# Kernel tuning notes

Measured on AMD Instinct MI355X. Metric: run time of the kernel, lower is better.

The kernel has to match this reference:

```python
import jax, jax.numpy as jnp
import numpy as np

GRID = 3


def setup_inputs() -> dict:
    key = jax.random.key(0)
    k1, k2, k3 = jax.random.split(key, 3)
    b, c, h, w = 8, 64, 128, 128
    h0, w0 = 64, 64
    x = jax.random.normal(k1, (b, c, h, w), dtype=jnp.float32)
    depth = jax.random.normal(k2, (b, GRID * 4 * c, h0, w0), dtype=jnp.float32)
    depth_ori = jax.random.uniform(k3, (b, 1, h, w), dtype=jnp.float32)
    return {"x": x, "depth": depth, "depth_ori": depth_ori}


def reference(x, depth, depth_ori):
    b, c, h, w = x.shape
    # self.dc = Sigmoid, then bilinear upsample (align_corners=False -> half-pixel,
    # matching jax.image.resize 'bilinear')
    d = jax.nn.sigmoid(depth)
    d = jax.image.resize(d, (b, d.shape[1], h, w), method="bilinear")
    d = d.reshape(b, GRID, 4 * c, h, w)
    # depth-weighted triangular interpolation weights, clamped at 0
    rd = jnp.arange(GRID, dtype=x.dtype).reshape(1, GRID, 1, 1)
    rd = jnp.maximum(1.0 - jnp.abs(rd - depth_ori * GRID), 0.0)  # (b, GRID, h, w)
    d = (d * rd[:, :, None]).sum(axis=1)            # (b, 4*c, h, w)
    d = d.reshape(b, 4, 4, c // 4, h, w)
    eye = jnp.eye(4, dtype=x.dtype).reshape(1, 4, 4, 1, 1, 1)
    mat = d + eye                                   # per-pixel 4x4 mixing matrix
    xr = x.reshape(b, 1, 4, c // 4, h, w)
    out = (mat * xr).sum(axis=2)                    # contract over inner 4-axis
    return out.reshape(b, c, h, w)
```

## Files before the change

### kernel.cpp

```cpp
#include <hip/hip_runtime.h>


__device__ __forceinline__ float sigmoid_fast(float v) {
    float e = __builtin_amdgcn_exp2f(v * -1.44269504088896340736f);
    return __builtin_amdgcn_rcpf(1.0f + e);
}

__global__ __launch_bounds__(256) void seblock_kernel(
    const float* __restrict__ x,
    const float* __restrict__ depth,
    const float* __restrict__ dori,
    float* __restrict__ out)
{
    const int t  = blockIdx.x * 256 + threadIdx.x;
    const int n  = t & 63;
    const int m  = (t >> 6) & 63;
    const int oc = (t >> 12) & 63;
    const int b  = t >> 18;
    const int i  = oc >> 4;
    const int k  = oc & 15;

    const int h0 = m << 1, w0 = n << 1;

    const int rm = (m > 0)  ? m - 1 : 0;
    const int rp = (m < 63) ? m + 1 : 63;

    float dv[3][4][3];
    #pragma unroll
    for (int g = 0; g < 3; ++g) {
        #pragma unroll
        for (int j = 0; j < 4; ++j) {
            const float* dp = depth + ((size_t)b * 768 + (g * 256 + i * 64 + j * 16 + k)) * 4096 + n;
            dv[g][j][0] = dp[rm * 64];
            dv[g][j][1] = dp[m  * 64];
            dv[g][j][2] = dp[rp * 64];
        }
    }

    const float* dop = dori + ((size_t)b * 128 + h0) * 128 + w0;
    const float2 q0 = *reinterpret_cast<const float2*>(dop);
    const float2 q1 = *reinterpret_cast<const float2*>(dop + 128);
    const float z[4] = { q0.x * 3.0f, q0.y * 3.0f, q1.x * 3.0f, q1.y * 3.0f };

    float xs[4][4];
    #pragma unroll
    for (int j = 0; j < 4; ++j) {
        const float* xp = x + (((size_t)b * 64 + (j * 16 + k)) * 128 + h0) * 128 + w0;
        const float2 a = *reinterpret_cast<const float2*>(xp);
        const float2 c = *reinterpret_cast<const float2*>(xp + 128);
        xs[j][0] = a.x; xs[j][1] = a.y; xs[j][2] = c.x; xs[j][3] = c.y;
    }

    float acc[4] = { xs[i][0], xs[i][1], xs[i][2], xs[i][3] };

    #pragma unroll
    for (int g = 0; g < 3; ++g) {
        float rdw[4];
        #pragma unroll
        for (int p = 0; p < 4; ++p)
            rdw[p] = fmaxf(1.0f - fabsf((float)g - z[p]), 0.0f);

        #pragma unroll
        for (int j = 0; j < 4; ++j) {
            const float a0 = sigmoid_fast(dv[g][j][0]);
            const float a1 = sigmoid_fast(dv[g][j][1]);
            const float a2 = sigmoid_fast(dv[g][j][2]);

            const float vt = fmaf(0.25f, a0, 0.75f * a1);
            const float vb = fmaf(0.25f, a2, 0.75f * a1);

            const float vtm = __shfl_up(vt, 1);
            const float vtp = __shfl_down(vt, 1);
            const float vbm = __shfl_up(vb, 1);
            const float vbp = __shfl_down(vb, 1);

            const float u0 = fmaf(0.25f, vtm, 0.75f * vt);
            const float u1 = fmaf(0.25f, vtp, 0.75f * vt);
            const float u2 = fmaf(0.25f, vbm, 0.75f * vb);
            const float u3 = fmaf(0.25f, vbp, 0.75f * vb);

            acc[0] = fmaf(rdw[0] * u0, xs[j][0], acc[0]);
            acc[1] = fmaf(rdw[1] * u1, xs[j][1], acc[1]);
            acc[2] = fmaf(rdw[2] * u2, xs[j][2], acc[2]);
            acc[3] = fmaf(rdw[3] * u3, xs[j][3], acc[3]);
        }
    }

    float* op = out + (((size_t)b * 64 + oc) * 128 + h0) * 128 + w0;
    *reinterpret_cast<float2*>(op)       = make_float2(acc[0], acc[1]);
    *reinterpret_cast<float2*>(op + 128) = make_float2(acc[2], acc[3]);
}

extern "C" void kernel_launch(void* const* d_in, const int* in_sizes, int n_in,
                              void* d_out, int out_size, void* d_ws, size_t ws_size,
                              hipStream_t stream) {
    const float* x     = (const float*)d_in[0];
    const float* depth = (const float*)d_in[1];
    const float* dori  = (const float*)d_in[2];
    float* out = (float*)d_out;

    seblock_kernel<<<8192, 256, 0, stream>>>(x, depth, dori, out);
}
```

Baseline: 183.7 us.

## Slide each wave down 8 rows, reusing sigmoids and using packed half math

Each wavefront now handles 8 consecutive low-res rows for one channel/batch. It keeps sigmoid values for three depth rows in registers and slides the window, so each depth row is loaded and passed through sigmoid once instead of three times. The next row is prefetched while the current one is computed. Vertical and horizontal interpolation run in packed fp16 with half the shuffles, and the grid drops from 8192 to 1024 blocks with a min-occupancy launch bound. The fp16 interpolation adds rounding error, and fewer blocks plus higher register pressure may limit latency hiding.

```diff
diff --git a/kernel.cpp b/kernel.cpp
--- a/kernel.cpp
+++ b/kernel.cpp
@@ -1,4 +1,5 @@
 #include <hip/hip_runtime.h>
+#include <hip/hip_fp16.h>
 
 
 __device__ __forceinline__ float sigmoid_fast(float v) {
@@ -6,89 +7,118 @@
     return __builtin_amdgcn_rcpf(1.0f + e);
 }
 
-__global__ __launch_bounds__(256) void seblock_kernel(
+#define NCH 12
+
+__global__ __launch_bounds__(256, 4) void seblock_kernel(
     const float* __restrict__ x,
     const float* __restrict__ depth,
     const float* __restrict__ dori,
     float* __restrict__ out)
 {
-    const int t  = blockIdx.x * 256 + threadIdx.x;
-    const int n  = t & 63;
-    const int m  = (t >> 6) & 63;
-    const int oc = (t >> 12) & 63;
-    const int b  = t >> 18;
+    const int lane = threadIdx.x & 63;
+    const int wsub = __builtin_amdgcn_readfirstlane(threadIdx.x >> 6);
+    const int wid  = (blockIdx.x << 2) | wsub;
+    const int mt = wid & 7;
+    const int oc = (wid >> 3) & 63;
+    const int b  = wid >> 9;
     const int i  = oc >> 4;
     const int k  = oc & 15;
+    const int m0 = mt << 3;
 
-    const int h0 = m << 1, w0 = n << 1;
+    int cofs[NCH];
+    #pragma unroll
+    for (int g = 0; g < 3; ++g)
+        #pragma unroll
+        for (int j = 0; j < 4; ++j)
+            cofs[g * 4 + j] = (b * 768 + g * 256 + i * 64 + j * 16 + k) * 4096;
 
-    const int rm = (m > 0)  ? m - 1 : 0;
-    const int rp = (m < 63) ? m + 1 : 63;
+    auto rowoff = [](int r) { return ((r < 0) ? 0 : (r > 63 ? 63 : r)) * 64; };
 
-    float dv[3][4][3];
+    float rawA[NCH], rawB[NCH], raw[NCH];
+    {
+        const int rA = rowoff(m0 - 1), rB = rowoff(m0), rC = rowoff(m0 + 1);
+        #pragma unroll
+        for (int c = 0; c < NCH; ++c) rawA[c] = depth[cofs[c] + rA + lane];
+        #pragma unroll
+        for (int c = 0; c < NCH; ++c) rawB[c] = depth[cofs[c] + rB + lane];
+        #pragma unroll
+        for (int c = 0; c < NCH; ++c) raw[c]  = depth[cofs[c] + rC + lane];
+    }
+
+    float sA[NCH], sB[NCH], sC[NCH];
     #pragma unroll
-    for (int g = 0; g < 3; ++g) {
+    for (int c = 0; c < NCH; ++c) sA[c] = sigmoid_fast(rawA[c]);
+    #pragma unroll
+    for (int c = 0; c < NCH; ++c) sB[c] = sigmoid_fast(rawB[c]);
+
+    const int xk   = (b * 64 + k) * 16384;
+    const int dob  = b * 16384;
+    const int outb = (b * 64 + oc) * 16384;
+    const int ln2  = 2 * lane;
+
+    const __half2 c25 = __float2half2_rn(0.25f);
+    const __half2 c75 = __float2half2_rn(0.75f);
+
+    #pragma unroll
+    for (int t = 0; t < 8; ++t) {
+        const int m = m0 + t;
+        const int h0off = (m << 1) * 128;
+
+        float xs[4][4];
         #pragma unroll
         for (int j = 0; j < 4; ++j) {
-            const float* dp = depth + ((size_t)b * 768 + (g * 256 + i * 64 + j * 16 + k)) * 4096 + n;
-            dv[g][j][0] = dp[rm * 64];
-            dv[g][j][1] = dp[m  * 64];
-            dv[g][j][2] = dp[rp * 64];
+            const float2 a  = *reinterpret_cast<const float2*>(x + xk + j * 262144 + h0off + ln2);
+            const float2 c2 = *reinterpret_cast<const float2*>(x + xk + j * 262144 + h0off + 128 + ln2);
+            xs[j][0] = a.x; xs[j][1] = a.y; xs[j][2] = c2.x; xs[j][3] = c2.y;
         }
-    }
-
-    const float* dop = dori + ((size_t)b * 128 + h0) * 128 + w0;
-    const float2 q0 = *reinterpret_cast<const float2*>(dop);
-    const float2 q1 = *reinterpret_cast<const float2*>(dop + 128);
-    const float z[4] = { q0.x * 3.0f, q0.y * 3.0f, q1.x * 3.0f, q1.y * 3.0f };
-
-    float xs[4][4];
-    #pragma unroll
-    for (int j = 0; j < 4; ++j) {
-        const float* xp = x + (((size_t)b * 64 + (j * 16 + k)) * 128 + h0) * 128 + w0;
-        const float2 a = *reinterpret_cast<const float2*>(xp);
-        const float2 c = *reinterpret_cast<const float2*>(xp + 128);
-        xs[j][0] = a.x; xs[j][1] = a.y; xs[j][2] = c.x; xs[j][3] = c.y;
-    }
-
-    float acc[4] = { xs[i][0], xs[i][1], xs[i][2], xs[i][3] };
-
-    #pragma unroll
-    for (int g = 0; g < 3; ++g) {
-        float rdw[4];
-        #pragma unroll
-        for (int p = 0; p < 4; ++p)
-            rdw[p] = fmaxf(1.0f - fabsf((float)g - z[p]), 0.0f);
+        const float2 q0 = *reinterpret_cast<const float2*>(dori + dob + h0off + ln2);
+        const float2 q1 = *reinterpret_cast<const float2*>(dori + dob + h0off + 128 + ln2);
 
         #pragma unroll
-        for (int j = 0; j < 4; ++j) {
-            const float a0 = sigmoid_fast(dv[g][j][0]);
-            const float a1 = sigmoid_fast(dv[g][j][1]);
-            const float a2 = sigmoid_fast(dv[g][j][2]);
+        for (int c = 0; c < NCH; ++c) sC[c] = sigmoid_fast(raw[c]);
 
-            const float vt = fmaf(0.25f, a0, 0.75f * a1);
-            const float vb = fmaf(0.25f, a2, 0.75f * a1);
+        if (t < 7) {
+            const int rN = rowoff(m + 2);
+            #pragma unroll
+            for (int c = 0; c < NCH; ++c) raw[c] = depth[cofs[c] + rN + lane];
+        }
 
-            const float vtm = __shfl_up(vt, 1);
-            const float vtp = __shfl_down(vt, 1);
-            const float vbm = __shfl_up(vb, 1);
-            const float vbp = __shfl_down(vb, 1);
+        const float z0 = q0.x * 3.0f, z1 = q0.y * 3.0f, z2 = q1.x * 3.0f, z3 = q1.y * 3.0f;
 
-            const float u0 = fmaf(0.25f, vtm, 0.75f * vt);
-            const float u1 = fmaf(0.25f, vtp, 0.75f * vt);
-            const float u2 = fmaf(0.25f, vbm, 0.75f * vb);
-            const float u3 = fmaf(0.25f, vbp, 0.75f * vb);
+        float acc0 = xs[i][0], acc1 = xs[i][1], acc2 = xs[i][2], acc3 = xs[i][3];
+        #pragma unroll
+        for (int g = 0; g < 3; ++g) {
+            float d0 = 0.0f, d1 = 0.0f, d2 = 0.0f, d3 = 0.0f;
+            #pragma unroll
+            for (int j = 0; j < 4; ++j) {
+                const int c = g * 4 + j;
+                const __half2 a02 = __floats2half2_rn(sA[c], sC[c]);
+                const __half2 a11 = __float2half2_rn(sB[c]);
+                const __half2 vtb = __hfma2(a02, c25, __hmul2(a11, c75));
+                const int vi = __builtin_bit_cast(int, vtb);
+                const __half2 vm = __builtin_bit_cast(__half2, __shfl_up(vi, 1));
+                const __half2 vp = __builtin_bit_cast(__half2, __shfl_down(vi, 1));
+                const __half2 tt  = __hmul2(vtb, c75);
+                const __half2 u02 = __hfma2(vm, c25, tt);
+                const __half2 u13 = __hfma2(vp, c25, tt);
+                d0 = fmaf(__low2float(u02),  xs[j][0], d0);
+                d1 = fmaf(__low2float(u13),  xs[j][1], d1);
+                d2 = fmaf(__high2float(u02), xs[j][2], d2);
+                d3 = fmaf(__high2float(u13), xs[j][3], d3);
+            }
+            const float gf = (float)g;
+            acc0 = fmaf(fmaxf(1.0f - fabsf(gf - z0), 0.0f), d0, acc0);
+            acc1 = fmaf(fmaxf(1.0f - fabsf(gf - z1), 0.0f), d1, acc1);
+            acc2 = fmaf(fmaxf(1.0f - fabsf(gf - z2), 0.0f), d2, acc2);
+            acc3 = fmaf(fmaxf(1.0f - fabsf(gf - z3), 0.0f), d3, acc3);
+        }
 
-            acc[0] = fmaf(rdw[0] * u0, xs[j][0], acc[0]);
-            acc[1] = fmaf(rdw[1] * u1, xs[j][1], acc[1]);
-            acc[2] = fmaf(rdw[2] * u2, xs[j][2], acc[2]);
-            acc[3] = fmaf(rdw[3] * u3, xs[j][3], acc[3]);
-        }
+        *reinterpret_cast<float2*>(out + outb + h0off + ln2)       = make_float2(acc0, acc1);
+        *reinterpret_cast<float2*>(out + outb + h0off + 128 + ln2) = make_float2(acc2, acc3);
+
+        #pragma unroll
+        for (int c = 0; c < NCH; ++c) { sA[c] = sB[c]; sB[c] = sC[c]; }
     }
-
-    float* op = out + (((size_t)b * 64 + oc) * 128 + h0) * 128 + w0;
-    *reinterpret_cast<float2*>(op)       = make_float2(acc[0], acc[1]);
-    *reinterpret_cast<float2*>(op + 128) = make_float2(acc[2], acc[3]);
 }
 
 extern "C" void kernel_launch(void* const* d_in, const int* in_sizes, int n_in,
@@ -99,5 +129,5 @@
     const float* dori  = (const float*)d_in[2];
     float* out = (float*)d_out;
 
-    seblock_kernel<<<8192, 256, 0, stream>>>(x, depth, dori, out);
+    seblock_kernel<<<1024, 256, 0, stream>>>(x, depth, dori, out);
 }
```

New measurement: 185.7 us. No clear change (+1.1%).
